# Performance work log

Hardware: AMD Instinct MI355X
Metric: run time of the kernel (lower is better)

Reference implementation:

```python
import jax, jax.numpy as jnp
import numpy as np

N = 1_000_000   # active voxels
C_IN = 32
C_OUT = 32
K = 27          # 3x3x3 kernel volume


def setup_inputs() -> dict:
    key = jax.random.key(0)
    k1, k2, k3, k4, k5 = jax.random.split(key, 5)
    in_feature = jax.random.normal(k1, (N, C_IN), dtype=jnp.float32)
    # torch init: uniform(-std, std), std = 1/sqrt(in_channels * kernel_volume)
    std = 1.0 / np.sqrt(C_IN * K)
    weight = jax.random.uniform(k2, (K, C_IN, C_OUT), jnp.float32, -std, std)
    bias = jax.random.uniform(k3, (C_OUT,), jnp.float32, -std, std)
    # kernel map: for each kernel offset k and each output voxel n, the index of
    # the contributing input voxel, plus a validity mask (sparse neighborhoods)
    kmap_idx = jax.random.randint(k4, (K, N), 0, N, dtype=jnp.int32)
    kmap_valid = jax.random.randint(k5, (K, N), 0, 2, dtype=jnp.int32).astype(bool)
    # center tap of a stride-1 sparse conv always maps voxel to itself
    kmap_idx = kmap_idx.at[K // 2].set(jnp.arange(N, dtype=jnp.int32))
    kmap_valid = kmap_valid.at[K // 2].set(True)
    return {
        "in_feature": in_feature,
        "weight": weight,
        "bias": bias,
        "kmap_idx": kmap_idx,
        "kmap_valid": kmap_valid,
    }


def reference(in_feature, weight, bias, kmap_idx, kmap_valid):
    # Gather-GEMM-scatter sparse conv: out[n] = sum_k W[k]^T @ x[kmap[k,n]] (if valid) + b
    # Loop over the 27 kernel taps (fixed kernel volume) to avoid materializing
    # the full [N, 27, C_in] gathered tensor.
    n_out = kmap_idx.shape[1]
    out = jnp.zeros((n_out, weight.shape[2]), dtype=in_feature.dtype)
    for k in range(weight.shape[0]):
        g = in_feature[kmap_idx[k]] * kmap_valid[k][:, None].astype(in_feature.dtype)
        out = out + jnp.einsum("nc,cd->nd", g, weight[k])
    return out + bias
```

## Files before the change

### kernel.cpp

```cpp
#include <hip/hip_runtime.h>
#include <stdint.h>

#define KVOL 27
#define CIN  32
#define COUT 32

typedef short bf16x8 __attribute__((ext_vector_type(8)));
typedef float f32x4  __attribute__((ext_vector_type(4)));

__global__ void detect_valid_layout(const uint8_t* __restrict__ valid_bytes,
                                    int* __restrict__ flag) {
    __shared__ int s_sum;
    if (threadIdx.x == 0) s_sum = 0;
    __syncthreads();
    int local = 0;
    for (int g = threadIdx.x; g < 1024; g += 256) {
        local += valid_bytes[4 * g + 1] + valid_bytes[4 * g + 2] + valid_bytes[4 * g + 3];
    }
    atomicAdd(&s_sum, local);
    __syncthreads();
    if (threadIdx.x == 0) flag[0] = (s_sum == 0) ? 1 : 0;
}

__device__ inline unsigned short f2bf(float f) {
    unsigned int u = __float_as_uint(f);
    return (unsigned short)((u + 0x7fffu + ((u >> 16) & 1u)) >> 16);
}

__global__ __launch_bounds__(256)
void convert_x(const float* __restrict__ X, short* __restrict__ Xb, int n8) {
    int i = blockIdx.x * blockDim.x + threadIdx.x;
    if (i < 4) {
        bf16x8 z = {};
        *((bf16x8*)Xb + (size_t)n8 + i) = z;
    }
    if (i >= n8) return;
    const float4* p = (const float4*)X + 2 * (size_t)i;
    float4 f0 = p[0], f1 = p[1];
    bf16x8 o;
    o[0] = (short)f2bf(f0.x); o[1] = (short)f2bf(f0.y);
    o[2] = (short)f2bf(f0.z); o[3] = (short)f2bf(f0.w);
    o[4] = (short)f2bf(f1.x); o[5] = (short)f2bf(f1.y);
    o[6] = (short)f2bf(f1.z); o[7] = (short)f2bf(f1.w);
    *((bf16x8*)Xb + (size_t)i) = o;
}

__global__ __launch_bounds__(256)
void convert_w(const float* __restrict__ W, short* __restrict__ Wt) {
    int i = blockIdx.x * blockDim.x + threadIdx.x;
    if (i >= KVOL * CIN * COUT) return;
    int k  = i >> 10;
    int co = (i >> 5) & 31;
    int ci = i & 31;
    Wt[i] = (short)f2bf(W[k * 1024 + ci * 32 + co]);
}

__global__ __launch_bounds__(256)
void sparse_conv_mfma(const short* __restrict__ Xb,
                      const short* __restrict__ Wt,
                      const float* __restrict__ bias,
                      const int* __restrict__ idx,
                      const uint8_t* __restrict__ validb,
                      const int* __restrict__ flag,
                      float* __restrict__ out, int N) {
    const int lane = threadIdx.x & 63;
    const int wave = threadIdx.x >> 6;
    const int col  = lane & 15;
    const int quad = lane >> 4;
    const int base = blockIdx.x * 256 + wave * 64;

    __shared__ int s_idx[4][KVOL * 64];
    int* sw = &s_idx[wave][0];

    const bool int_layout = (flag[0] != 0);
    const int* validi = (const int*)validb;

    const int r = base + lane;
    if (r < N) {
        if (int_layout) {
#pragma unroll
            for (int kc = 0; kc < KVOL; kc += 9) {
                int j[9], v[9];
#pragma unroll
                for (int t = 0; t < 9; ++t) j[t] = idx[(size_t)(kc + t) * N + r];
#pragma unroll
                for (int t = 0; t < 9; ++t) v[t] = validi[(size_t)(kc + t) * N + r];
#pragma unroll
                for (int t = 0; t < 9; ++t) sw[(kc + t) * 64 + lane] = v[t] ? j[t] : N;
            }
        } else {
#pragma unroll
            for (int kc = 0; kc < KVOL; kc += 9) {
                int j[9], v[9];
#pragma unroll
                for (int t = 0; t < 9; ++t) j[t] = idx[(size_t)(kc + t) * N + r];
#pragma unroll
                for (int t = 0; t < 9; ++t) v[t] = (int)validb[(size_t)(kc + t) * N + r];
#pragma unroll
                for (int t = 0; t < 9; ++t) sw[(kc + t) * 64 + lane] = v[t] ? j[t] : N;
            }
        }
    } else {
#pragma unroll
        for (int k = 0; k < KVOL; ++k) sw[k * 64 + lane] = N;
    }

    f32x4 acc[4][2] = {};
    bf16x8 a0[4], a1[4];

    auto gather = [&](bf16x8 (&a)[4], int k) {
#pragma unroll
        for (int g = 0; g < 4; ++g) {
            const int j = sw[k * 64 + g * 16 + col];
            a[g] = *(const bf16x8*)(Xb + (size_t)j * CIN + quad * 8);
        }
    };
    auto tap = [&](bf16x8 (&a)[4], int k) {
        const bf16x8 b0 = *(const bf16x8*)(Wt + (k * 1024 + col * 32 + quad * 8));
        const bf16x8 b1 = *(const bf16x8*)(Wt + (k * 1024 + (col + 16) * 32 + quad * 8));
#pragma unroll
        for (int g = 0; g < 4; ++g) {
            acc[g][0] = __builtin_amdgcn_mfma_f32_16x16x32_bf16(a[g], b0, acc[g][0], 0, 0, 0);
            acc[g][1] = __builtin_amdgcn_mfma_f32_16x16x32_bf16(a[g], b1, acc[g][1], 0, 0, 0);
        }
    };

    gather(a0, 0);
#pragma unroll 1
    for (int kk = 0; kk < (KVOL - 1) / 2; ++kk) {
        const int k = kk * 2;
        gather(a1, k + 1);
        tap(a0, k);
        gather(a0, k + 2);
        tap(a1, k + 1);
    }
    tap(a0, KVOL - 1);

    const float bv0 = bias[col];
    const float bv1 = bias[col + 16];
#pragma unroll
    for (int g = 0; g < 4; ++g) {
#pragma unroll
        for (int rr = 0; rr < 4; ++rr) {
            const int row = base + g * 16 + quad * 4 + rr;
            if (row < N) {
                out[(size_t)row * COUT + col]      = acc[g][0][rr] + bv0;
                out[(size_t)row * COUT + col + 16] = acc[g][1][rr] + bv1;
            }
        }
    }
}

__global__ __launch_bounds__(256)
void sparse_conv_fp32(const float* __restrict__ X,
                      const float* __restrict__ W,
                      const float* __restrict__ B,
                      const int* __restrict__ idx,
                      const uint8_t* __restrict__ validb,
                      const int* __restrict__ flag,
                      float* __restrict__ out,
                      int N) {
    const int n = blockIdx.x * blockDim.x + threadIdx.x;
    if (n >= N) return;
    const bool int_layout = (flag[0] != 0);
    const int* validi = (const int*)validb;
    float acc[COUT];
#pragma unroll
    for (int co = 0; co < COUT; ++co) acc[co] = B[co];
    for (int k = 0; k < KVOL; ++k) {
        const size_t kn = (size_t)k * (size_t)N + (size_t)n;
        const int v = int_layout ? validi[kn] : (int)validb[kn];
        if (v) {
            const int j = idx[kn];
            const float4* xp = (const float4*)(X + (size_t)j * CIN);
            float xr[CIN];
#pragma unroll
            for (int q = 0; q < 8; ++q) {
                float4 t = xp[q];
                xr[4 * q + 0] = t.x; xr[4 * q + 1] = t.y;
                xr[4 * q + 2] = t.z; xr[4 * q + 3] = t.w;
            }
            const float* __restrict__ Wk = W + k * CIN * COUT;
#pragma unroll
            for (int ci = 0; ci < CIN; ++ci) {
                const float xv = xr[ci];
#pragma unroll
                for (int co = 0; co < COUT; ++co) acc[co] += xv * Wk[ci * COUT + co];
            }
        }
    }
    float4* op = (float4*)(out + (size_t)n * COUT);
#pragma unroll
    for (int q = 0; q < 8; ++q)
        op[q] = make_float4(acc[4 * q + 0], acc[4 * q + 1], acc[4 * q + 2], acc[4 * q + 3]);
}

extern "C" void kernel_launch(void* const* d_in, const int* in_sizes, int n_in,
                              void* d_out, int out_size, void* d_ws, size_t ws_size,
                              hipStream_t stream) {
    const float*   X      = (const float*)d_in[0];
    const float*   W      = (const float*)d_in[1];
    const float*   B      = (const float*)d_in[2];
    const int*     idx    = (const int*)d_in[3];
    const uint8_t* validb = (const uint8_t*)d_in[4];

    const int N = in_sizes[0] / CIN;

    const size_t xb_bytes = (size_t)(N + 1) * CIN * sizeof(short);
    const size_t wt_bytes = (size_t)KVOL * CIN * COUT * sizeof(short);
    const size_t need     = xb_bytes + wt_bytes + 256;

    if (ws_size >= need) {
        short* Xb  = (short*)d_ws;
        short* Wt  = (short*)((char*)d_ws + xb_bytes);
        int*   flag = (int*)((char*)d_ws + xb_bytes + wt_bytes);

        detect_valid_layout<<<1, 256, 0, stream>>>(validb, flag);

        const int n8 = (N * CIN) / 8;
        convert_x<<<(n8 + 255) / 256, 256, 0, stream>>>(X, Xb, n8);
        convert_w<<<(KVOL * CIN * COUT + 255) / 256, 256, 0, stream>>>(W, Wt);

        const int blocks = (N + 255) / 256;
        sparse_conv_mfma<<<blocks, 256, 0, stream>>>(Xb, Wt, B, idx, validb,
                                                     flag, (float*)d_out, N);
    } else {
        int* flag = (int*)d_ws;
        detect_valid_layout<<<1, 256, 0, stream>>>(validb, flag);
        const int blocks = (N + 255) / 256;
        sparse_conv_fp32<<<blocks, 256, 0, stream>>>(X, W, B, idx, validb,
                                                     flag, (float*)d_out, N);
    }
}
```

Measured before the change: 576.3 us.

## Stage kernel map in 9-tap chunks with vectorized nontemporal loads and higher occupancy

The kernel map is staged into shared memory in three chunks of 9 taps instead of all 27 at once, which shrinks per-wave LDS use from 27*64 to 9*64 ints. Index and validity loads become 16-byte vectorized nontemporal loads for full tiles, with a scalar fallback for tail tiles. Launch bounds now request 8 blocks per CU, and the gather address math uses a 32-bit shift. The aim is more resident waves to hide gather latency and fewer map-load instructions, at the cost of a pipeline restart (stage plus two prologue gathers) at each chunk boundary.

```diff
diff --git a/kernel.cpp b/kernel.cpp
--- a/kernel.cpp
+++ b/kernel.cpp
@@ -4,9 +4,12 @@
 #define KVOL 27
 #define CIN  32
 #define COUT 32
+#define CHUNK 9
+#define NCHUNK 3
 
 typedef short bf16x8 __attribute__((ext_vector_type(8)));
 typedef float f32x4  __attribute__((ext_vector_type(4)));
+typedef int   i32x4  __attribute__((ext_vector_type(4)));
 
 __global__ void detect_valid_layout(const uint8_t* __restrict__ valid_bytes,
                                     int* __restrict__ flag) {
@@ -55,7 +58,7 @@
     Wt[i] = (short)f2bf(W[k * 1024 + ci * 32 + co]);
 }
 
-__global__ __launch_bounds__(256)
+__global__ __launch_bounds__(256, 8)
 void sparse_conv_mfma(const short* __restrict__ Xb,
                       const short* __restrict__ Wt,
                       const float* __restrict__ bias,
@@ -69,50 +72,79 @@
     const int quad = lane >> 4;
     const int base = blockIdx.x * 256 + wave * 64;
 
-    __shared__ int s_idx[4][KVOL * 64];
+    __shared__ int s_idx[4][CHUNK * 64];
     int* sw = &s_idx[wave][0];
 
     const bool int_layout = (flag[0] != 0);
     const int* validi = (const int*)validb;
-
-    const int r = base + lane;
-    if (r < N) {
-        if (int_layout) {
-#pragma unroll
-            for (int kc = 0; kc < KVOL; kc += 9) {
-                int j[9], v[9];
-#pragma unroll
-                for (int t = 0; t < 9; ++t) j[t] = idx[(size_t)(kc + t) * N + r];
-#pragma unroll
-                for (int t = 0; t < 9; ++t) v[t] = validi[(size_t)(kc + t) * N + r];
-#pragma unroll
-                for (int t = 0; t < 9; ++t) sw[(kc + t) * 64 + lane] = v[t] ? j[t] : N;
-            }
-        } else {
-#pragma unroll
-            for (int kc = 0; kc < KVOL; kc += 9) {
-                int j[9], v[9];
-#pragma unroll
-                for (int t = 0; t < 9; ++t) j[t] = idx[(size_t)(kc + t) * N + r];
-#pragma unroll
-                for (int t = 0; t < 9; ++t) v[t] = (int)validb[(size_t)(kc + t) * N + r];
-#pragma unroll
-                for (int t = 0; t < 9; ++t) sw[(kc + t) * 64 + lane] = v[t] ? j[t] : N;
-            }
-        }
-    } else {
-#pragma unroll
-        for (int k = 0; k < KVOL; ++k) sw[k * 64 + lane] = N;
-    }
+    const char* XbB = (const char*)Xb;
+
+    const bool full = ((base + 64) <= N) && ((N & 3) == 0);
 
     f32x4 acc[4][2] = {};
     bf16x8 a0[4], a1[4];
 
-    auto gather = [&](bf16x8 (&a)[4], int k) {
+    auto stage = [&](int k0) {
+        if (full) {
+            if (int_layout) {
+#pragma unroll
+                for (int i = 0; i < 3; ++i) {
+                    const int s = i * 64 + lane;
+                    if (s < CHUNK * 16) {
+                        const int t  = s >> 4;
+                        const int c4 = (s & 15) << 2;
+                        const size_t off = (size_t)(k0 + t) * N + base + c4;
+                        i32x4 jv = __builtin_nontemporal_load((const i32x4*)(idx + off));
+                        i32x4 vv = __builtin_nontemporal_load((const i32x4*)(validi + off));
+                        i32x4 m;
+                        m[0] = vv[0] ? jv[0] : N;
+                        m[1] = vv[1] ? jv[1] : N;
+                        m[2] = vv[2] ? jv[2] : N;
+                        m[3] = vv[3] ? jv[3] : N;
+                        *(i32x4*)&sw[t * 64 + c4] = m;
+                    }
+                }
+            } else {
+#pragma unroll
+                for (int i = 0; i < 3; ++i) {
+                    const int s = i * 64 + lane;
+                    if (s < CHUNK * 16) {
+                        const int t  = s >> 4;
+                        const int c4 = (s & 15) << 2;
+                        const size_t off = (size_t)(k0 + t) * N + base + c4;
+                        i32x4 jv = __builtin_nontemporal_load((const i32x4*)(idx + off));
+                        unsigned vb = __builtin_nontemporal_load(
+                            (const unsigned*)(validb + off));
+                        i32x4 m;
+                        m[0] = (vb & 0x000000ffu) ? jv[0] : N;
+                        m[1] = (vb & 0x0000ff00u) ? jv[1] : N;
+                        m[2] = (vb & 0x00ff0000u) ? jv[2] : N;
+                        m[3] = (vb & 0xff000000u) ? jv[3] : N;
+                        *(i32x4*)&sw[t * 64 + c4] = m;
+                    }
+                }
+            }
+        } else {
+            const int r = base + lane;
+#pragma unroll
+            for (int t = 0; t < CHUNK; ++t) {
+                int m = N;
+                if (r < N) {
+                    const size_t off = (size_t)(k0 + t) * N + r;
+                    const int v = int_layout ? validi[off] : (int)validb[off];
+                    const int j = idx[off];
+                    m = v ? j : N;
+                }
+                sw[t * 64 + lane] = m;
+            }
+        }
+    };
+
+    auto gather = [&](bf16x8 (&a)[4], int lt) {
 #pragma unroll
         for (int g = 0; g < 4; ++g) {
-            const int j = sw[k * 64 + g * 16 + col];
-            a[g] = *(const bf16x8*)(Xb + (size_t)j * CIN + quad * 8);
+            const unsigned j = (unsigned)sw[lt * 64 + g * 16 + col];
+            a[g] = *(const bf16x8*)(XbB + ((size_t)((unsigned)(j << 6))) + quad * 16);
         }
     };
     auto tap = [&](bf16x8 (&a)[4], int k) {
@@ -125,16 +157,22 @@
         }
     };
 
-    gather(a0, 0);
 #pragma unroll 1
-    for (int kk = 0; kk < (KVOL - 1) / 2; ++kk) {
-        const int k = kk * 2;
-        gather(a1, k + 1);
-        tap(a0, k);
-        gather(a0, k + 2);
-        tap(a1, k + 1);
-    }
-    tap(a0, KVOL - 1);
+    for (int c = 0; c < NCHUNK; ++c) {
+        const int k0 = c * CHUNK;
+        stage(k0);
+        gather(a0, 0);
+        gather(a1, 1);
+        tap(a0, k0 + 0); gather(a0, 2);
+        tap(a1, k0 + 1); gather(a1, 3);
+        tap(a0, k0 + 2); gather(a0, 4);
+        tap(a1, k0 + 3); gather(a1, 5);
+        tap(a0, k0 + 4); gather(a0, 6);
+        tap(a1, k0 + 5); gather(a1, 7);
+        tap(a0, k0 + 6); gather(a0, 8);
+        tap(a1, k0 + 7);
+        tap(a0, k0 + 8);
+    }
 
     const float bv0 = bias[col];
     const float bv1 = bias[col + 16];
```

Measured after the change: 744.4 us. +29.2%, slower.
